# Performance work log

Measured on AMD Instinct MI355X. Metric: run time of the kernel, lower is better.

The kernel has to match this reference:

```python
import jax, jax.numpy as jnp
import numpy as np

B, T, C, H = 256, 256, 384, 64
MAX_REL = 3  # max_relative_position hardcoded in module


def setup_inputs() -> dict:
    key = jax.random.key(0)
    ks = jax.random.split(key, 6)
    s = 1.0 / np.sqrt(C)
    return {
        "x": jax.random.normal(ks[0], (B, T, C), dtype=jnp.float32),
        "Wq": jax.random.normal(ks[1], (C, H), dtype=jnp.float32) * s,
        "Wk": jax.random.normal(ks[2], (C, H), dtype=jnp.float32) * s,
        "Wv": jax.random.normal(ks[3], (C, H), dtype=jnp.float32) * s,
        "rel_k_table": jax.random.normal(ks[4], (2 * MAX_REL + 1, H), dtype=jnp.float32) * s,
        "rel_v_table": jax.random.normal(ks[5], (2 * MAX_REL + 1, H), dtype=jnp.float32) * s,
    }


def reference(x, Wq, Wk, Wv, rel_k_table, rel_v_table):
    Bd, Td, Cd = x.shape
    Hd = Wq.shape[1]
    q = x @ Wq  # [B,T,H]
    k = x @ Wk
    v = x @ Wv
    # relative position indices, clipped Shaw-style
    r = jnp.arange(Td)
    idx = jnp.clip(r[None, :] - r[:, None], -MAX_REL, MAX_REL) + MAX_REL  # [T,T]
    rk = rel_k_table[idx]  # [T,T,H]
    rv = rel_v_table[idx]  # [T,T,H]
    attn1 = jnp.einsum('bth,bsh->bts', q, k)
    attn2 = jnp.einsum('bth,tsh->bts', q, rk)
    scale = jnp.sqrt(jnp.asarray(Hd, dtype=x.dtype))
    scores = (attn1 + attn2) / scale
    causal = jnp.tril(jnp.ones((Td, Td), dtype=bool))
    scores = jnp.where(causal[None, :, :], scores, -jnp.inf)
    attn = jax.nn.softmax(scores, axis=-1)  # dropout = identity (eval mode)
    w1 = jnp.einsum('bts,bsh->bth', attn, v)
    w2 = jnp.einsum('bts,tsh->bth', attn, rv)
    return w1 + w2  # [B,T,H]
```

## Files before the change

kernel.cpp:

```cpp
#include <hip/hip_runtime.h>
#include <hip/hip_bf16.h>


typedef __attribute__((ext_vector_type(8))) __bf16 bf16x8;
typedef __attribute__((ext_vector_type(8))) short short8;
typedef __attribute__((ext_vector_type(4))) float f32x4;
typedef __attribute__((ext_vector_type(4))) int   i32x4;

#define MFMA16(A, B, C) __builtin_amdgcn_mfma_f32_16x16x32_bf16((A), (B), (C), 0, 0, 0)

__device__ __forceinline__ unsigned short f2bf(float f) {
    unsigned int u = __builtin_bit_cast(unsigned int, f);
    u = (u + 0x7FFFu + ((u >> 16) & 1u)) >> 16;
    return (unsigned short)u;
}
__device__ __forceinline__ float bf2f(unsigned short s) {
    unsigned int u = ((unsigned int)s) << 16;
    return __builtin_bit_cast(float, u);
}
__device__ __forceinline__ bf16x8 ld16(const unsigned short* p) {
    return __builtin_bit_cast(bf16x8, *(const i32x4*)p);
}

__global__ void prep_wt(const float* __restrict__ Wq, const float* __restrict__ Wk,
                        const float* __restrict__ Wv, const float* __restrict__ relk,
                        unsigned short* __restrict__ Wt, unsigned short* __restrict__ Rk) {
    int i = blockIdx.x * 256 + threadIdx.x;
    if (i < 3 * 64 * 384) {
        int kk = i % 384;
        int h  = (i / 384) & 63;
        int w  = i / (384 * 64);
        const float* W = (w == 0) ? Wq : ((w == 1) ? Wk : Wv);
        Wt[i] = f2bf(W[kk * 64 + h]);
    } else if (i < 3 * 64 * 384 + 1024) {
        int j = i - 3 * 64 * 384;
        int n = j >> 6, h = j & 63;
        Rk[j] = (n < 4) ? f2bf(relk[n * 64 + h]) : (unsigned short)0;
    }
}

__global__ __launch_bounds__(512, 1) void fused_kernel(
        const float* __restrict__ x, const unsigned short* __restrict__ Wt,
        const unsigned short* __restrict__ Rk, const float* __restrict__ relv,
        float* __restrict__ out) {
    extern __shared__ unsigned short sh[];
    unsigned short* ksh = sh;
    unsigned short* vTs = sh + 18432;
    unsigned short* qs  = sh + 35328;
    unsigned short* wc  = sh + 53760;

    const int tid  = threadIdx.x;
    const int wave = tid >> 6;
    const int lane = tid & 63;
    const int c    = lane & 15;
    const int quad = lane >> 4;
    const int b    = blockIdx.x;

    const f32x4 zero = {0.f, 0.f, 0.f, 0.f};

    const float* xbase = x + (size_t)(b * 256 + wave * 32 + c) * 384 + quad * 8;

    f32x4 aq[2][4], ak[2][4], av[2][4];
#pragma unroll
    for (int rt = 0; rt < 2; rt++)
#pragma unroll
        for (int nt = 0; nt < 4; nt++) { aq[rt][nt] = zero; ak[rt][nt] = zero; av[rt][nt] = zero; }

    f32x4 tmp[2][8];
#pragma unroll
    for (int rt = 0; rt < 2; rt++)
#pragma unroll
        for (int j = 0; j < 4; j++) {
            const float* xp = xbase + rt * 6144 + j * 32;
            tmp[rt][2 * j]     = *(const f32x4*)xp;
            tmp[rt][2 * j + 1] = *(const f32x4*)(xp + 4);
        }

#pragma unroll
    for (int ck = 0; ck < 3; ck++) {
        if (ck) __syncthreads();
#pragma unroll
        for (int it = 0; it < 6; it++) {
            int P_ = it * 512 + tid;
            int r = P_ >> 4, pc = P_ & 15;
            i32x4 d = *(const i32x4*)(Wt + r * 384 + ck * 128 + pc * 8);
            *(i32x4*)(wc + r * 136 + pc * 8) = d;
        }
        __syncthreads();

        bf16x8 a[2][4];
#pragma unroll
        for (int rt = 0; rt < 2; rt++)
#pragma unroll
            for (int j = 0; j < 4; j++) {
                short8 xs8;
#pragma unroll
                for (int e = 0; e < 4; e++) {
                    xs8[e]     = (short)f2bf(tmp[rt][2 * j][e]);
                    xs8[4 + e] = (short)f2bf(tmp[rt][2 * j + 1][e]);
                }
                a[rt][j] = __builtin_bit_cast(bf16x8, xs8);
            }
        if (ck < 2) {
#pragma unroll
            for (int rt = 0; rt < 2; rt++)
#pragma unroll
                for (int j = 0; j < 4; j++) {
                    const float* xp = xbase + rt * 6144 + (ck + 1) * 128 + j * 32;
                    tmp[rt][2 * j]     = *(const f32x4*)xp;
                    tmp[rt][2 * j + 1] = *(const f32x4*)(xp + 4);
                }
        }

#pragma unroll
        for (int j = 0; j < 4; j++) {
            const int col = j * 32 + quad * 8;
#pragma unroll
            for (int nt = 0; nt < 4; nt++) {
                bf16x8 bq = ld16(wc + (nt * 16 + c) * 136 + col);
                bf16x8 bk = ld16(wc + (64 + nt * 16 + c) * 136 + col);
                bf16x8 aw = ld16(wc + (128 + nt * 16 + c) * 136 + col);
                aq[0][nt] = MFMA16(a[0][j], bq, aq[0][nt]);
                aq[1][nt] = MFMA16(a[1][j], bq, aq[1][nt]);
                ak[0][nt] = MFMA16(a[0][j], bk, ak[0][nt]);
                ak[1][nt] = MFMA16(a[1][j], bk, ak[1][nt]);
                av[0][nt] = MFMA16(aw, a[0][j], av[0][nt]);
                av[1][nt] = MFMA16(aw, a[1][j], av[1][nt]);
            }
        }
    }

#pragma unroll
    for (int rt = 0; rt < 2; rt++)
#pragma unroll
        for (int nt = 0; nt < 4; nt++)
#pragma unroll
            for (int r = 0; r < 4; r++) {
                int row = wave * 32 + rt * 16 + quad * 4 + r;
                qs[row * 72 + nt * 16 + c]  = f2bf(aq[rt][nt][r]);
                ksh[row * 72 + nt * 16 + c] = f2bf(ak[rt][nt][r]);
                vTs[(nt * 16 + quad * 4 + r) * 264 + wave * 32 + rt * 16 + c] = f2bf(av[rt][nt][r]);
            }
    __syncthreads();

    const int tA = wave, tB = 15 - wave;
    bf16x8 qA0 = ld16(qs + (tA * 16 + c) * 72 + quad * 8);
    bf16x8 qA1 = ld16(qs + (tA * 16 + c) * 72 + 32 + quad * 8);
    bf16x8 qB0 = ld16(qs + (tB * 16 + c) * 72 + quad * 8);
    bf16x8 qB1 = ld16(qs + (tB * 16 + c) * 72 + 32 + quad * 8);
    float rv[4][4];
#pragma unroll
    for (int j = 0; j < 4; j++)
#pragma unroll
        for (int nt = 0; nt < 4; nt++) rv[j][nt] = relv[j * 64 + nt * 16 + c];
    __syncthreads();

    unsigned short* Pw = sh + 35328 + wave * 4224;

#pragma unroll
    for (int it2 = 0; it2 < 2; it2++) {
        const int tt  = it2 ? tB : tA;
        const bf16x8 aq0 = it2 ? qB0 : qA0;
        const bf16x8 aq1 = it2 ? qB1 : qA1;
        const int nst = tt + 1;

        f32x4 e = zero;
        e = MFMA16(aq0, ld16(Rk + c * 64 + quad * 8), e);
        e = MFMA16(aq1, ld16(Rk + c * 64 + 32 + quad * 8), e);
        float ef[4][4];
#pragma unroll
        for (int r = 0; r < 4; r++)
#pragma unroll
            for (int n = 0; n < 4; n++)
                ef[r][n] = __shfl(e[r], (lane & 48) + n, 64);

        __asm__ __volatile__("s_waitcnt lgkmcnt(0)" ::: "memory");

        float l[4] = {0.f, 0.f, 0.f, 0.f};
#pragma unroll
        for (int st = 0; st < 16; st++) {
            if (st < nst) {
                const unsigned short* kp = ksh + (st * 16 + c) * 72 + quad * 8;
                f32x4 s = zero;
                s = MFMA16(aq0, ld16(kp), s);
                s = MFMA16(aq1, ld16(kp + 32), s);
#pragma unroll
                for (int r = 0; r < 4; r++) {
                    int tg = tt * 16 + quad * 4 + r;
                    int sg = st * 16 + c;
                    int d  = sg - tg;
                    float ee = (d <= -3) ? ef[r][0] : (d == -2) ? ef[r][1]
                             : (d == -1) ? ef[r][2] : ef[r][3];
                    float p = (d > 0) ? 0.f : __expf(0.125f * (s[r] + ee));
                    l[r] += p;
                    Pw[(quad * 4 + r) * 264 + sg] = f2bf(p);
                }
            }
        }
        if (nst & 1) {
#pragma unroll
            for (int r = 0; r < 4; r++) Pw[(quad * 4 + r) * 264 + nst * 16 + c] = 0;
        }
#pragma unroll
        for (int r = 0; r < 4; r++)
#pragma unroll
            for (int ofs = 1; ofs < 16; ofs <<= 1)
                l[r] += __shfl_xor(l[r], ofs, 64);
        float rl[4];
#pragma unroll
        for (int r = 0; r < 4; r++) rl[r] = 1.0f / l[r];

        __asm__ __volatile__("s_waitcnt lgkmcnt(0)" ::: "memory");

        f32x4 o[4];
#pragma unroll
        for (int nt = 0; nt < 4; nt++) o[nt] = zero;
        const int ksteps = (nst + 1) >> 1;
#pragma unroll
        for (int ks = 0; ks < 8; ks++) {
            if (ks < ksteps) {
                bf16x8 ap = ld16(Pw + c * 264 + ks * 32 + quad * 8);
#pragma unroll
                for (int nt = 0; nt < 4; nt++) {
                    bf16x8 bv = ld16(vTs + (nt * 16 + c) * 264 + ks * 32 + quad * 8);
                    o[nt] = MFMA16(ap, bv, o[nt]);
                }
            }
        }

#pragma unroll
        for (int r = 0; r < 4; r++) {
            int tl = quad * 4 + r;
            int tg = tt * 16 + tl;
            float pa  = (tg >= 2) ? bf2f(Pw[tl * 264 + tg - 2]) * rl[r] : 0.f;
            float pb  = (tg >= 1) ? bf2f(Pw[tl * 264 + tg - 1]) * rl[r] : 0.f;
            float pcv = bf2f(Pw[tl * 264 + tg]) * rl[r];
#pragma unroll
            for (int nt = 0; nt < 4; nt++) {
                float r0 = rv[0][nt];
                float w2 = r0 + pa * (rv[1][nt] - r0) + pb * (rv[2][nt] - r0)
                              + pcv * (rv[3][nt] - r0);
                out[(size_t)(b * 256 + tg) * 64 + nt * 16 + c] = o[nt][r] * rl[r] + w2;
            }
        }
    }
}

extern "C" void kernel_launch(void* const* d_in, const int* in_sizes, int n_in,
                              void* d_out, int out_size, void* d_ws, size_t ws_size,
                              hipStream_t stream) {
    const float* x    = (const float*)d_in[0];
    const float* Wq   = (const float*)d_in[1];
    const float* Wk   = (const float*)d_in[2];
    const float* Wv   = (const float*)d_in[3];
    const float* relk = (const float*)d_in[4];
    const float* relv = (const float*)d_in[5];
    float* out = (float*)d_out;

    char* ws = (char*)d_ws;
    unsigned short* Wt = (unsigned short*)(ws);
    unsigned short* Rk = (unsigned short*)(ws + 147456);

    (void)hipFuncSetAttribute((const void*)fused_kernel,
                              hipFuncAttributeMaxDynamicSharedMemorySize, 159744);

    prep_wt<<<292, 256, 0, stream>>>(Wq, Wk, Wv, relk, Wt, Rk);
    fused_kernel<<<256, 512, 159744, stream>>>(x, Wt, Rk, relv, out);
}
```

Before: 197.0 us.

## Double waves per block, splitting key tiles and head columns across wave pairs

Raises the fused kernel from 8 to 16 waves per block. Each wave now projects 16 rows instead of 32. In attention, two waves share one query tile: they split the key tiles by parity and the output head columns into halves, and combine the partial softmax denominators through shared memory. The aim is more latency hiding within the single resident block per CU, at the cost of extra block-wide barriers and cross-wave exchange of P and the row sums.

```diff
diff --git a/kernel.cpp b/kernel.cpp
--- a/kernel.cpp
+++ b/kernel.cpp
@@ -39,7 +39,7 @@
     }
 }
 
-__global__ __launch_bounds__(512, 1) void fused_kernel(
+__global__ __launch_bounds__(1024, 1) void fused_kernel(
         const float* __restrict__ x, const unsigned short* __restrict__ Wt,
         const unsigned short* __restrict__ Rk, const float* __restrict__ relv,
         float* __restrict__ out) {
@@ -48,6 +48,7 @@
     unsigned short* vTs = sh + 18432;
     unsigned short* qs  = sh + 35328;
     unsigned short* wc  = sh + 53760;
+    float* lsum = (float*)(sh + 69120);
 
     const int tid  = threadIdx.x;
     const int wave = tid >> 6;
@@ -58,58 +59,49 @@
 
     const f32x4 zero = {0.f, 0.f, 0.f, 0.f};
 
-    const float* xbase = x + (size_t)(b * 256 + wave * 32 + c) * 384 + quad * 8;
-
-    f32x4 aq[2][4], ak[2][4], av[2][4];
-#pragma unroll
-    for (int rt = 0; rt < 2; rt++)
-#pragma unroll
-        for (int nt = 0; nt < 4; nt++) { aq[rt][nt] = zero; ak[rt][nt] = zero; av[rt][nt] = zero; }
-
-    f32x4 tmp[2][8];
-#pragma unroll
-    for (int rt = 0; rt < 2; rt++)
-#pragma unroll
-        for (int j = 0; j < 4; j++) {
-            const float* xp = xbase + rt * 6144 + j * 32;
-            tmp[rt][2 * j]     = *(const f32x4*)xp;
-            tmp[rt][2 * j + 1] = *(const f32x4*)(xp + 4);
-        }
+    const float* xbase = x + (size_t)(b * 256 + wave * 16 + c) * 384 + quad * 8;
+
+    f32x4 aq[4], ak[4], av[4];
+#pragma unroll
+    for (int nt = 0; nt < 4; nt++) { aq[nt] = zero; ak[nt] = zero; av[nt] = zero; }
+
+    f32x4 tmp[8];
+#pragma unroll
+    for (int j = 0; j < 4; j++) {
+        tmp[2 * j]     = *(const f32x4*)(xbase + j * 32);
+        tmp[2 * j + 1] = *(const f32x4*)(xbase + j * 32 + 4);
+    }
 
 #pragma unroll
     for (int ck = 0; ck < 3; ck++) {
         if (ck) __syncthreads();
 #pragma unroll
-        for (int it = 0; it < 6; it++) {
-            int P_ = it * 512 + tid;
+        for (int it = 0; it < 3; it++) {
+            int P_ = it * 1024 + tid;
             int r = P_ >> 4, pc = P_ & 15;
             i32x4 d = *(const i32x4*)(Wt + r * 384 + ck * 128 + pc * 8);
             *(i32x4*)(wc + r * 136 + pc * 8) = d;
         }
         __syncthreads();
 
-        bf16x8 a[2][4];
-#pragma unroll
-        for (int rt = 0; rt < 2; rt++)
+        bf16x8 a[4];
+#pragma unroll
+        for (int j = 0; j < 4; j++) {
+            short8 xs8;
+#pragma unroll
+            for (int e = 0; e < 4; e++) {
+                xs8[e]     = (short)f2bf(tmp[2 * j][e]);
+                xs8[4 + e] = (short)f2bf(tmp[2 * j + 1][e]);
+            }
+            a[j] = __builtin_bit_cast(bf16x8, xs8);
+        }
+        if (ck < 2) {
 #pragma unroll
             for (int j = 0; j < 4; j++) {
-                short8 xs8;
-#pragma unroll
-                for (int e = 0; e < 4; e++) {
-                    xs8[e]     = (short)f2bf(tmp[rt][2 * j][e]);
-                    xs8[4 + e] = (short)f2bf(tmp[rt][2 * j + 1][e]);
-                }
-                a[rt][j] = __builtin_bit_cast(bf16x8, xs8);
-            }
-        if (ck < 2) {
-#pragma unroll
-            for (int rt = 0; rt < 2; rt++)
-#pragma unroll
-                for (int j = 0; j < 4; j++) {
-                    const float* xp = xbase + rt * 6144 + (ck + 1) * 128 + j * 32;
-                    tmp[rt][2 * j]     = *(const f32x4*)xp;
-                    tmp[rt][2 * j + 1] = *(const f32x4*)(xp + 4);
-                }
+                const float* xp = xbase + (ck + 1) * 128 + j * 32;
+                tmp[2 * j]     = *(const f32x4*)xp;
+                tmp[2 * j + 1] = *(const f32x4*)(xp + 4);
+            }
         }
 
 #pragma unroll
@@ -120,42 +112,41 @@
                 bf16x8 bq = ld16(wc + (nt * 16 + c) * 136 + col);
                 bf16x8 bk = ld16(wc + (64 + nt * 16 + c) * 136 + col);
                 bf16x8 aw = ld16(wc + (128 + nt * 16 + c) * 136 + col);
-                aq[0][nt] = MFMA16(a[0][j], bq, aq[0][nt]);
-                aq[1][nt] = MFMA16(a[1][j], bq, aq[1][nt]);
-                ak[0][nt] = MFMA16(a[0][j], bk, ak[0][nt]);
-                ak[1][nt] = MFMA16(a[1][j], bk, ak[1][nt]);
-                av[0][nt] = MFMA16(aw, a[0][j], av[0][nt]);
-                av[1][nt] = MFMA16(aw, a[1][j], av[1][nt]);
-            }
-        }
-    }
-
-#pragma unroll
-    for (int rt = 0; rt < 2; rt++)
-#pragma unroll
-        for (int nt = 0; nt < 4; nt++)
-#pragma unroll
-            for (int r = 0; r < 4; r++) {
-                int row = wave * 32 + rt * 16 + quad * 4 + r;
-                qs[row * 72 + nt * 16 + c]  = f2bf(aq[rt][nt][r]);
-                ksh[row * 72 + nt * 16 + c] = f2bf(ak[rt][nt][r]);
-                vTs[(nt * 16 + quad * 4 + r) * 264 + wave * 32 + rt * 16 + c] = f2bf(av[rt][nt][r]);
-            }
+                aq[nt] = MFMA16(a[j], bq, aq[nt]);
+                ak[nt] = MFMA16(a[j], bk, ak[nt]);
+                av[nt] = MFMA16(aw, a[j], av[nt]);
+            }
+        }
+    }
+
+#pragma unroll
+    for (int nt = 0; nt < 4; nt++)
+#pragma unroll
+        for (int r = 0; r < 4; r++) {
+            int row = wave * 16 + quad * 4 + r;
+            qs[row * 72 + nt * 16 + c]  = f2bf(aq[nt][r]);
+            ksh[row * 72 + nt * 16 + c] = f2bf(ak[nt][r]);
+            vTs[(nt * 16 + quad * 4 + r) * 264 + wave * 16 + c] = f2bf(av[nt][r]);
+        }
     __syncthreads();
 
-    const int tA = wave, tB = 15 - wave;
+    const int p  = wave & 7;
+    const int hi = wave >> 3;
+    const int tA = p, tB = 15 - p;
+
     bf16x8 qA0 = ld16(qs + (tA * 16 + c) * 72 + quad * 8);
     bf16x8 qA1 = ld16(qs + (tA * 16 + c) * 72 + 32 + quad * 8);
     bf16x8 qB0 = ld16(qs + (tB * 16 + c) * 72 + quad * 8);
     bf16x8 qB1 = ld16(qs + (tB * 16 + c) * 72 + 32 + quad * 8);
-    float rv[4][4];
+    float rv[4][2];
 #pragma unroll
     for (int j = 0; j < 4; j++)
 #pragma unroll
-        for (int nt = 0; nt < 4; nt++) rv[j][nt] = relv[j * 64 + nt * 16 + c];
+        for (int i = 0; i < 2; i++)
+            rv[j][i] = relv[j * 64 + (hi * 2 + i) * 16 + c];
     __syncthreads();
 
-    unsigned short* Pw = sh + 35328 + wave * 4224;
+    unsigned short* Pw = sh + 35328 + p * 4224;
 
 #pragma unroll
     for (int it2 = 0; it2 < 2; it2++) {
@@ -174,56 +165,61 @@
             for (int n = 0; n < 4; n++)
                 ef[r][n] = __shfl(e[r], (lane & 48) + n, 64);
 
-        __asm__ __volatile__("s_waitcnt lgkmcnt(0)" ::: "memory");
-
         float l[4] = {0.f, 0.f, 0.f, 0.f};
 #pragma unroll
         for (int st = 0; st < 16; st++) {
-            if (st < nst) {
-                const unsigned short* kp = ksh + (st * 16 + c) * 72 + quad * 8;
-                f32x4 s = zero;
-                s = MFMA16(aq0, ld16(kp), s);
-                s = MFMA16(aq1, ld16(kp + 32), s);
-#pragma unroll
-                for (int r = 0; r < 4; r++) {
-                    int tg = tt * 16 + quad * 4 + r;
-                    int sg = st * 16 + c;
-                    int d  = sg - tg;
-                    float ee = (d <= -3) ? ef[r][0] : (d == -2) ? ef[r][1]
-                             : (d == -1) ? ef[r][2] : ef[r][3];
-                    float p = (d > 0) ? 0.f : __expf(0.125f * (s[r] + ee));
-                    l[r] += p;
-                    Pw[(quad * 4 + r) * 264 + sg] = f2bf(p);
+            if ((st & 1) == hi) {
+                if (st < nst) {
+                    const unsigned short* kp = ksh + (st * 16 + c) * 72 + quad * 8;
+                    f32x4 s = zero;
+                    s = MFMA16(aq0, ld16(kp), s);
+                    s = MFMA16(aq1, ld16(kp + 32), s);
+#pragma unroll
+                    for (int r = 0; r < 4; r++) {
+                        int tg = tt * 16 + quad * 4 + r;
+                        int sg = st * 16 + c;
+                        int d  = sg - tg;
+                        float ee = (d <= -3) ? ef[r][0] : (d == -2) ? ef[r][1]
+                                 : (d == -1) ? ef[r][2] : ef[r][3];
+                        float pv = (d > 0) ? 0.f : __expf(0.125f * (s[r] + ee));
+                        l[r] += pv;
+                        Pw[(quad * 4 + r) * 264 + sg] = f2bf(pv);
+                    }
+                } else if (st == nst && (nst & 1)) {
+#pragma unroll
+                    for (int r = 0; r < 4; r++)
+                        Pw[(quad * 4 + r) * 264 + st * 16 + c] = 0;
                 }
             }
-        }
-        if (nst & 1) {
-#pragma unroll
-            for (int r = 0; r < 4; r++) Pw[(quad * 4 + r) * 264 + nst * 16 + c] = 0;
         }
 #pragma unroll
         for (int r = 0; r < 4; r++)
 #pragma unroll
             for (int ofs = 1; ofs < 16; ofs <<= 1)
                 l[r] += __shfl_xor(l[r], ofs, 64);
+        if (c == 0) {
+#pragma unroll
+            for (int r = 0; r < 4; r++)
+                lsum[(p * 2 + hi) * 16 + quad * 4 + r] = l[r];
+        }
+        __syncthreads();
         float rl[4];
 #pragma unroll
-        for (int r = 0; r < 4; r++) rl[r] = 1.0f / l[r];
-
-        __asm__ __volatile__("s_waitcnt lgkmcnt(0)" ::: "memory");
-
-        f32x4 o[4];
-#pragma unroll
-        for (int nt = 0; nt < 4; nt++) o[nt] = zero;
+        for (int r = 0; r < 4; r++)
+            rl[r] = 1.0f / (l[r] + lsum[(p * 2 + (1 - hi)) * 16 + quad * 4 + r]);
+
+        f32x4 o[2];
+        o[0] = zero; o[1] = zero;
         const int ksteps = (nst + 1) >> 1;
 #pragma unroll
         for (int ks = 0; ks < 8; ks++) {
             if (ks < ksteps) {
                 bf16x8 ap = ld16(Pw + c * 264 + ks * 32 + quad * 8);
 #pragma unroll
-                for (int nt = 0; nt < 4; nt++) {
+                for (int i = 0; i < 2; i++) {
+                    const int nt = hi * 2 + i;
                     bf16x8 bv = ld16(vTs + (nt * 16 + c) * 264 + ks * 32 + quad * 8);
-                    o[nt] = MFMA16(ap, bv, o[nt]);
+                    o[i] = MFMA16(ap, bv, o[i]);
                 }
             }
         }
@@ -236,13 +232,15 @@
             float pb  = (tg >= 1) ? bf2f(Pw[tl * 264 + tg - 1]) * rl[r] : 0.f;
             float pcv = bf2f(Pw[tl * 264 + tg]) * rl[r];
 #pragma unroll
-            for (int nt = 0; nt < 4; nt++) {
-                float r0 = rv[0][nt];
-                float w2 = r0 + pa * (rv[1][nt] - r0) + pb * (rv[2][nt] - r0)
-                              + pcv * (rv[3][nt] - r0);
-                out[(size_t)(b * 256 + tg) * 64 + nt * 16 + c] = o[nt][r] * rl[r] + w2;
-            }
-        }
+            for (int i = 0; i < 2; i++) {
+                const int nt = hi * 2 + i;
+                float r0 = rv[0][i];
+                float w2 = r0 + pa * (rv[1][i] - r0) + pb * (rv[2][i] - r0)
+                              + pcv * (rv[3][i] - r0);
+                out[(size_t)(b * 256 + tg) * 64 + nt * 16 + c] = o[i][r] * rl[r] + w2;
+            }
+        }
+        __syncthreads();
     }
 }
 
@@ -265,5 +263,5 @@
                               hipFuncAttributeMaxDynamicSharedMemorySize, 159744);
 
     prep_wt<<<292, 256, 0, stream>>>(Wq, Wk, Wv, relk, Wt, Rk);
-    fused_kernel<<<256, 512, 159744, stream>>>(x, Wt, Rk, relv, out);
-}
+    fused_kernel<<<256, 1024, 159744, stream>>>(x, Wt, Rk, relv, out);
+}
```

Measured after the change: 198.0 us. About the same (+0.5%).
